# Performance work log

Measured on AMD Instinct MI355X. Metric: run time of the kernel, lower is better.

The kernel has to match this reference:

```python
import jax, jax.numpy as jnp
import numpy as np

B, D, F, E, G = 2048, 1024, 4096, 16, 2
EPS = 1e-9
LN_EPS = 1e-5


def setup_inputs() -> dict:
    key = jax.random.key(0)
    ks = jax.random.split(key, 10)
    s_in = 1.0 / np.sqrt(D)
    s_out = 1.0 / np.sqrt(F)
    return {
        "cycle_curve_data": jax.random.normal(ks[0], (B, D), jnp.float32),
        "logits": jax.random.normal(ks[1], (B, E), jnp.float32),
        "moe_masks": jax.random.randint(ks[2], (B, E), 0, 2, jnp.int32),
        "ew_in": jax.random.uniform(ks[3], (E, D, F), jnp.float32, -s_in, s_in),
        "ew_out": jax.random.uniform(ks[4], (E, F, D), jnp.float32, -s_out, s_out),
        "eb_out": jax.random.uniform(ks[5], (E, D), jnp.float32, -s_out, s_out),
        "gw_in": jax.random.uniform(ks[6], (G, D, F), jnp.float32, -s_in, s_in),
        "gw_out": jax.random.uniform(ks[7], (G, F, D), jnp.float32, -s_out, s_out),
        "gb_out": jax.random.uniform(ks[8], (G, D), jnp.float32, -s_out, s_out),
        "ln_gamma": jnp.ones((D,), jnp.float32),
        "ln_beta": jnp.zeros((D,), jnp.float32),
    }


def _moe_forward(x, logits, moe_masks, ew_in, ew_out, eb_out, gw_in, gw_out, gb_out, ln_gamma, ln_beta):
    b = x.shape[0]
    mask = (moe_masks == 1).astype(logits.dtype)          # [B,E]
    raw = jax.nn.softmax(logits, axis=1)                   # [B,E]
    gates = raw * mask
    gates = gates / (jnp.sum(gates, axis=1, keepdims=True) + EPS)
    # Per-expert MLPBlockGELU over all tokens; gate=0 zeroes out non-dispatched
    # tokens exactly as MOEDispatcher.combine does.
    h = jax.nn.gelu(jnp.einsum('bd,edf->ebf', x, ew_in), approximate=False)  # [E,B,F]
    eout = jnp.einsum('ebf,efd->ebd', h, ew_out) + eb_out[:, None, :]        # [E,B,D]
    moe_out = jnp.einsum('be,ebd->bd', gates, eout).astype(jnp.bfloat16)     # combine + bf16 cast
    # general experts (dense, added to routed output; bf16+f32 promotes to f32)
    gh = jax.nn.gelu(jnp.einsum('bd,gdf->gbf', x, gw_in), approximate=False)
    gout = jnp.einsum('gbf,gfd->gbd', gh, gw_out) + gb_out[:, None, :]       # [G,B,D]
    final = jnp.sum(gout, axis=0) + moe_out                                  # f32
    # residual + LayerNorm
    y = final + x
    mu = jnp.mean(y, axis=-1, keepdims=True)
    var = jnp.mean(jnp.square(y - mu), axis=-1, keepdims=True)
    final_out = (y - mu) * jax.lax.rsqrt(var + LN_EPS) * ln_gamma + ln_beta
    # training losses
    expert_logits = jnp.mean(raw, axis=0)                                    # [E]
    expert_sample_count = jnp.sum((gates != 0).astype(raw.dtype), axis=0) / b
    aug_loss = jnp.mean(expert_logits * expert_sample_count)
    s = jnp.sum(raw * mask) / b
    guide_loss = (1.0 - s) * (1.0 - s)
    return final_out, aug_loss, guide_loss


def reference(cycle_curve_data, logits, moe_masks, ew_in, ew_out, eb_out, gw_in, gw_out, gb_out, ln_gamma, ln_beta):
    return _moe_forward(cycle_curve_data, logits, moe_masks, ew_in, ew_out, eb_out,
                        gw_in, gw_out, gb_out, ln_gamma, ln_beta)
```

## Files before the change

kernel.cpp:

```cpp
#include <hip/hip_runtime.h>
#include <hip/hip_bf16.h>

#define B_TOK 2048
#define DDIM 1024
#define FDIM 4096
#define NE 16
#define NG 2
#define BD ((long)B_TOK * DDIM)

typedef unsigned short u16;
typedef __attribute__((ext_vector_type(8))) short bf16x8;
typedef __attribute__((ext_vector_type(4))) float f32x4;

__device__ inline u16 f2bf(float x) {
  union { float f; unsigned u; } v; v.f = x;
  return (u16)((v.u + 0x7fffu + ((v.u >> 16) & 1u)) >> 16);
}
__device__ inline float bfround(float x) {
  union { float f; unsigned u; } v; v.f = x;
  v.u = ((v.u + 0x7fffu + ((v.u >> 16) & 1u)) >> 16) << 16;
  return v.f;
}
__device__ inline float fast_erf(float x) {
  float ax = fabsf(x);
  float t = __builtin_amdgcn_rcpf(1.0f + 0.3275911f * ax);
  float poly = t * (0.254829592f + t * (-0.284496736f + t * (1.421413741f +
               t * (-1.453152027f + t * 1.061405429f))));
  float r = 1.0f - poly * __expf(-ax * ax);
  return copysignf(r, x);
}
__device__ inline float gelu_exact(float x) {
  return 0.5f * x * (1.0f + fast_erf(x * 0.70710678118654752440f));
}
__device__ inline void gload16(const void* g, void* l) {
  __builtin_amdgcn_global_load_lds((const __attribute__((address_space(1))) void*)g,
                                   (__attribute__((address_space(3))) void*)l, 16, 0, 0);
}
__device__ inline float waveSum(float v) {
  v += __shfl_down(v, 32); v += __shfl_down(v, 16); v += __shfl_down(v, 8);
  v += __shfl_down(v, 4);  v += __shfl_down(v, 2);  v += __shfl_down(v, 1);
  return v;
}

__global__ __launch_bounds__(256) void gating_kernel(
    const float* __restrict__ logits, const int* __restrict__ masks,
    float* __restrict__ gates, float* __restrict__ loss)
{
  const int b = blockIdx.x * 256 + threadIdx.x;
  const int lane = threadIdx.x & 63;
  const float* lr = logits + (long)b * NE;
  const int*   mr = masks  + (long)b * NE;
  float raw[NE]; int mk[NE];
  float mx = -1e30f;
#pragma unroll
  for (int e = 0; e < NE; ++e) { raw[e] = lr[e]; mx = fmaxf(mx, raw[e]); }
  float s = 0.f;
#pragma unroll
  for (int e = 0; e < NE; ++e) { raw[e] = expf(raw[e] - mx); s += raw[e]; }
  float inv = 1.0f / s;
#pragma unroll
  for (int e = 0; e < NE; ++e) raw[e] *= inv;
  float gs = 0.f;
#pragma unroll
  for (int e = 0; e < NE; ++e) { mk[e] = (mr[e] == 1); gs += mk[e] ? raw[e] : 0.f; }
  float ginv = 1.0f / (gs + 1e-9f);
  float* gr = gates + (long)b * NE;
#pragma unroll
  for (int e = 0; e < NE; ++e) gr[e] = (mk[e] ? raw[e] : 0.f) * ginv;
#pragma unroll
  for (int e = 0; e < NE; ++e) {
    float cs = waveSum(raw[e]);
    float cc = waveSum(mk[e] ? 1.f : 0.f);
    if (lane == 0) { atomicAdd(&loss[e], cs); atomicAdd(&loss[NE + e], cc); }
  }
  float t = waveSum(gs);
  if (lane == 0) atomicAdd(&loss[32], t);
}

__global__ void finalize_loss(const float* __restrict__ loss, float* __restrict__ out2) {
  if (threadIdx.x == 0) {
    float aug = 0.f;
    for (int e = 0; e < NE; ++e)
      aug += (loss[e] / (float)B_TOK) * (loss[NE + e] / (float)B_TOK);
    aug *= (1.0f / NE);
    float s = loss[32] / (float)B_TOK;
    out2[0] = aug;
    out2[1] = (1.f - s) * (1.f - s);
  }
}

__global__ __launch_bounds__(256) void compact_kernel(
    const int* __restrict__ masks, int* __restrict__ tok,
    int* __restrict__ pos, int* __restrict__ cnts)
{
  const int e = blockIdx.x, tid = threadIdx.x;
  const int lane = tid & 63, wave = tid >> 6;
  __shared__ int wcnt[4];
  __shared__ int runbase;
  if (tid == 0) runbase = 0;
  __syncthreads();
  for (int b0 = 0; b0 < B_TOK; b0 += 256) {
    int b = b0 + tid;
    int m = (masks[(long)b * NE + e] == 1);
    unsigned long long bal = __ballot(m);
    int pre = __popcll(bal & ((1ull << lane) - 1ull));
    if (lane == 0) wcnt[wave] = __popcll(bal);
    __syncthreads();
    int base = runbase;
    for (int w = 0; w < wave; ++w) base += wcnt[w];
    if (m) {
      int p = base + pre;
      tok[(e << 11) + p] = b;
      pos[(long)b * NE + e] = p;
    } else {
      pos[(long)b * NE + e] = -1;
    }
    __syncthreads();
    if (tid == 0) runbase += wcnt[0] + wcnt[1] + wcnt[2] + wcnt[3];
    __syncthreads();
  }
  const int cnt = runbase;
  const int cnt_pad = (cnt + 127) & ~127;
  for (int i = cnt + tid; i < cnt_pad; i += 256)
    tok[(e << 11) + i] = 0;
  if (tid == 0) { cnts[e] = cnt; cnts[NE + e] = cnt_pad; }
}

__global__ __launch_bounds__(256) void cvt_x_kernel(const float* __restrict__ x, u16* __restrict__ xb) {
  long i = ((long)blockIdx.x * 256 + threadIdx.x) * 4;
  float4 v = *(const float4*)&x[i];
  ushort4 o; o.x = f2bf(v.x); o.y = f2bf(v.y); o.z = f2bf(v.z); o.w = f2bf(v.w);
  *(ushort4*)&xb[i] = o;
}

__global__ __launch_bounds__(256) void bias_init_kernel(
    const float* __restrict__ gates, const float* __restrict__ eb,
    const float* __restrict__ gb, float* __restrict__ moe_bias, float* __restrict__ gen_p)
{
  long i = (long)blockIdx.x * 256 + threadIdx.x;
  int b = (int)(i >> 10), d = (int)(i & 1023);
  const float* gr = gates + (long)b * NE;
  float s = 0.f;
#pragma unroll
  for (int e = 0; e < NE; ++e) s += gr[e] * eb[e * DDIM + d];
  moe_bias[i] = s;
  gen_p[i] = gb[d] + gb[DDIM + d];
#pragma unroll
  for (int sl = 1; sl < 8; ++sl) gen_p[sl * BD + i] = 0.f;
}

__global__ __launch_bounds__(256) void transpose_cvt(
    const float* __restrict__ src, u16* __restrict__ dst,
    int R, int C, long sZ, long dZ)
{
  __shared__ float t[64][65];
  const float* s = src + (long)blockIdx.z * sZ;
  u16* d = dst + (long)blockIdx.z * dZ;
  const int c0 = blockIdx.x * 64, r0 = blockIdx.y * 64;
  const int tid = threadIdx.x;
#pragma unroll
  for (int it = 0; it < 4; ++it) {
    int idx = tid + it * 256;
    int r = idx >> 4, cq = (idx & 15) * 4;
    float4 v = *(const float4*)&s[(long)(r0 + r) * C + c0 + cq];
    t[r][cq] = v.x; t[r][cq + 1] = v.y; t[r][cq + 2] = v.z; t[r][cq + 3] = v.w;
  }
  __syncthreads();
#pragma unroll
  for (int it = 0; it < 4; ++it) {
    int idx = tid + it * 256;
    int c = idx >> 4, rq = (idx & 15) * 4;
    ushort4 o;
    o.x = f2bf(t[rq][c]); o.y = f2bf(t[rq+1][c]); o.z = f2bf(t[rq+2][c]); o.w = f2bf(t[rq+3][c]);
    *(ushort4*)&d[(long)(c0 + c) * R + r0 + rq] = o;
  }
}

template<int MODE>
__global__ __launch_bounds__(256) void gemm128(
    const u16* __restrict__ A, int lda, long aZ,
    const u16* __restrict__ Bm, int ldb, long bZ,
    int klen,
    u16* __restrict__ H, long hZ,
    float* __restrict__ C, long cZ,
    const int* __restrict__ tok, const int* __restrict__ cnts, int ebase)
{
  int lin = ((int)blockIdx.z * gridDim.y + blockIdx.y) * gridDim.x + blockIdx.x;
  const int T = gridDim.x * gridDim.y * gridDim.z;
  lin = (lin & 7) * (T >> 3) + (lin >> 3);
  const int bx = lin % gridDim.x;
  const int rest = lin / gridDim.x;
  const int by = rest % gridDim.y;
  const int bz = rest / gridDim.y;

  const int zi = (MODE == 2) ? (bz >> 2) : bz;
  const int ks = (MODE == 2) ? (bz & 3) * klen : 0;
  const int m0 = by * 128, n0 = bx * 128;
  if (MODE != 2 && cnts && m0 >= cnts[NE + ebase + zi]) return;

  __shared__ u16 sA[2][128 * 32];
  __shared__ u16 sB[2][128 * 32];
  const u16* Az = A + (long)zi * aZ;
  const u16* Bz = Bm + (long)zi * bZ;
  const int tid = threadIdx.x, lane = tid & 63, wave = tid >> 6;

  const int off = tid * 16;
  const int sr  = off >> 6;
  const int ske = (off & 63) >> 1;
  int arow0 = m0 + sr, arow1 = m0 + sr + 64;
  if (MODE == 0 && tok) {
    const int* tz = tok + ((ebase + zi) << 11);
    arow0 = tz[arow0]; arow1 = tz[arow1];
  }
  const u16* gA0 = Az + (long)arow0 * lda + ks + ske;
  const u16* gA1 = Az + (long)arow1 * lda + ks + ske;
  const u16* gB0 = Bz + (long)(n0 + sr) * ldb + ks + ske;
  const u16* gB1 = gB0 + (long)64 * ldb;

  const int wr = wave >> 1, wc = wave & 1;
  const int fr = lane & 15, fk = (lane >> 4) * 8;
  const int rAo = (wr * 64 + fr) * 32 + fk;
  const int rBo = (wc * 64 + fr) * 32 + fk;

  f32x4 zero = {0.f, 0.f, 0.f, 0.f};
  f32x4 acc[4][4];
#pragma unroll
  for (int m = 0; m < 4; ++m)
#pragma unroll
    for (int n = 0; n < 4; ++n) acc[m][n] = zero;

  auto STAGE = [&](int buf, int kk) {
    gload16(gA0 + kk, &sA[buf][wave * 512]);
    gload16(gA1 + kk, &sA[buf][2048 + wave * 512]);
    gload16(gB0 + kk, &sB[buf][wave * 512]);
    gload16(gB1 + kk, &sB[buf][2048 + wave * 512]);
  };
  auto COMPUTE = [&](int buf) {
    bf16x8 av[4], bv[4];
#pragma unroll
    for (int m = 0; m < 4; ++m) av[m] = *(const bf16x8*)(&sA[buf][rAo + m * 512]);
#pragma unroll
    for (int n = 0; n < 4; ++n) bv[n] = *(const bf16x8*)(&sB[buf][rBo + n * 512]);
#pragma unroll
    for (int m = 0; m < 4; ++m)
#pragma unroll
      for (int n = 0; n < 4; ++n)
        acc[m][n] = __builtin_amdgcn_mfma_f32_16x16x32_bf16(av[m], bv[n], acc[m][n], 0, 0, 0);
  };

  const int nt = klen >> 5;
  STAGE(0, 0);
  __syncthreads();
  for (int t = 0; t < nt; t += 2) {
    STAGE(1, (t + 1) << 5);
    COMPUTE(0);
    __syncthreads();
    if (t + 2 < nt) STAGE(0, (t + 2) << 5);
    COMPUTE(1);
    __syncthreads();
  }

  const int er = m0 + wr * 64 + (lane >> 4) * 4;
  const int ec = n0 + wc * 64 + fr;
  if (MODE == 0) {
    u16* Hz = H + (long)zi * hZ;
#pragma unroll
    for (int m = 0; m < 4; ++m)
#pragma unroll
      for (int n = 0; n < 4; ++n) {
        f32x4 v = acc[m][n];
        int rb = er + m * 16, cb = ec + n * 16;
#pragma unroll
        for (int j = 0; j < 4; ++j)
          Hz[(long)(rb + j) * FDIM + cb] = f2bf(gelu_exact(v[j]));
      }
  } else if (MODE == 1) {
    float* Cz = C + (long)(ebase + zi) * cZ;
#pragma unroll
    for (int m = 0; m < 4; ++m)
#pragma unroll
      for (int n = 0; n < 4; ++n) {
        f32x4 v = acc[m][n];
        int rb = er + m * 16, cb = ec + n * 16;
#pragma unroll
        for (int j = 0; j < 4; ++j)
          Cz[(long)(rb + j) * DDIM + cb] = v[j];
      }
  } else {
    float* Cz = C + (long)bz * cZ;
#pragma unroll
    for (int m = 0; m < 4; ++m)
#pragma unroll
      for (int n = 0; n < 4; ++n) {
        f32x4 v = acc[m][n];
        int rb = er + m * 16, cb = ec + n * 16;
#pragma unroll
        for (int j = 0; j < 4; ++j)
          Cz[(long)(rb + j) * DDIM + cb] += v[j];
      }
  }
}

__global__ __launch_bounds__(256) void combine_ln_kernel(
    const float* __restrict__ x, const float* __restrict__ moe_bias,
    const float* __restrict__ Eout, const float* __restrict__ gen_p,
    const int* __restrict__ pos, const float* __restrict__ gates,
    const float* __restrict__ gamma, const float* __restrict__ beta,
    float* __restrict__ out)
{
  const int b = blockIdx.x, tid = threadIdx.x;
  const int lane = tid & 63, wave = tid >> 6;
  const long base = (long)b * DDIM;
  __shared__ int posr[NE];
  __shared__ float gr[NE];
  __shared__ float red[4];
  if (tid < NE) { posr[tid] = pos[(long)b * NE + tid]; gr[tid] = gates[(long)b * NE + tid]; }
  __syncthreads();
  float y[4];
  float ls = 0.f;
#pragma unroll
  for (int i = 0; i < 4; ++i) {
    int d = tid + i * 256;
    long idx = base + d;
    float moe = moe_bias[idx];
#pragma unroll
    for (int e = 0; e < NE; ++e) {
      int p = posr[e];
      if (p >= 0) moe += gr[e] * Eout[((long)e * B_TOK + p) * DDIM + d];
    }
    moe = bfround(moe);
    float ge = 0.f;
#pragma unroll
    for (int sl = 0; sl < 8; ++sl) ge += gen_p[(long)sl * BD + idx];
    y[i] = moe + ge + x[idx];
    ls += y[i];
  }
  float t = waveSum(ls);
  if (lane == 0) red[wave] = t;
  __syncthreads();
  float mean = (red[0] + red[1] + red[2] + red[3]) * (1.0f / DDIM);
  __syncthreads();
  float vs = 0.f;
#pragma unroll
  for (int i = 0; i < 4; ++i) { float d2 = y[i] - mean; vs += d2 * d2; }
  t = waveSum(vs);
  if (lane == 0) red[wave] = t;
  __syncthreads();
  float var = (red[0] + red[1] + red[2] + red[3]) * (1.0f / DDIM);
  float inv = rsqrtf(var + 1e-5f);
#pragma unroll
  for (int i = 0; i < 4; ++i) {
    int d = tid + i * 256;
    out[base + d] = (y[i] - mean) * inv * gamma[d] + beta[d];
  }
}

extern "C" void kernel_launch(void* const* d_in, const int* in_sizes, int n_in,
                              void* d_out, int out_size, void* d_ws, size_t ws_size,
                              hipStream_t stream)
{
  const float* x      = (const float*)d_in[0];
  const float* logits = (const float*)d_in[1];
  const int*   masks  = (const int*)d_in[2];
  const float* ew_in  = (const float*)d_in[3];
  const float* ew_out = (const float*)d_in[4];
  const float* eb_out = (const float*)d_in[5];
  const float* gw_in  = (const float*)d_in[6];
  const float* gw_out = (const float*)d_in[7];
  const float* gb_out = (const float*)d_in[8];
  const float* gamma  = (const float*)d_in[9];
  const float* beta   = (const float*)d_in[10];
  float* out = (float*)d_out;

  char* w = (char*)d_ws;
  size_t off = 0;
  auto alloc = [&](size_t bytes) -> void* {
    off = (off + 4095) & ~(size_t)4095;
    void* p = w + off; off += bytes; return p;
  };
  const long DF = (long)DDIM * FDIM;
  const long BF = (long)B_TOK * FDIM;

  float* gates    = (float*)alloc((size_t)B_TOK * NE * 4);
  float* loss     = (float*)alloc(64 * 4);
  int*   tok      = (int*)alloc((size_t)NE * B_TOK * 4);
  int*   pos      = (int*)alloc((size_t)B_TOK * NE * 4);
  int*   cnts     = (int*)alloc(2 * NE * 4);
  u16*   xb       = (u16*)alloc((size_t)BD * 2);
  float* moe_bias = (float*)alloc((size_t)BD * 4);
  float* gen_p    = (float*)alloc(8 * (size_t)BD * 4);
  float* Eout     = (float*)alloc((size_t)NE * BD * 4);
  u16*   WgInT    = (u16*)alloc((size_t)NG * DF * 2);
  u16*   WgOutT   = (u16*)alloc((size_t)NG * DF * 2);
  u16*   Hg       = (u16*)alloc((size_t)NG * BF * 2);

  const size_t per = 2 * (size_t)DF * 2 + (size_t)BF * 2 + 3 * 4096;
  int CE = 16;
  while (CE > 1 && off + (size_t)CE * per > ws_size) CE >>= 1;
  u16* WinT  = (u16*)alloc((size_t)CE * DF * 2);
  u16* WoutT = (u16*)alloc((size_t)CE * DF * 2);
  u16* Hb    = (u16*)alloc((size_t)CE * BF * 2);

  hipMemsetAsync(loss, 0, 64 * 4, stream);
  gating_kernel<<<8, 256, 0, stream>>>(logits, masks, gates, loss);
  finalize_loss<<<1, 64, 0, stream>>>(loss, out + BD);
  compact_kernel<<<NE, 256, 0, stream>>>(masks, tok, pos, cnts);
  cvt_x_kernel<<<2048, 256, 0, stream>>>(x, xb);
  bias_init_kernel<<<8192, 256, 0, stream>>>(gates, eb_out, gb_out, moe_bias, gen_p);

  for (int e0 = 0; e0 < NE; e0 += CE) {
    transpose_cvt<<<dim3(FDIM/64, DDIM/64, CE), 256, 0, stream>>>(
        ew_in + (long)e0 * DF, WinT, DDIM, FDIM, DF, DF);
    transpose_cvt<<<dim3(DDIM/64, FDIM/64, CE), 256, 0, stream>>>(
        ew_out + (long)e0 * DF, WoutT, FDIM, DDIM, DF, DF);
    gemm128<0><<<dim3(FDIM/128, B_TOK/128, CE), 256, 0, stream>>>(
        xb, DDIM, 0L, WinT, DDIM, DF, DDIM,
        Hb, BF, nullptr, 0L, tok, cnts, e0);
    gemm128<1><<<dim3(DDIM/128, B_TOK/128, CE), 256, 0, stream>>>(
        Hb, FDIM, BF, WoutT, FDIM, DF, FDIM,
        nullptr, 0L, Eout, BD, nullptr, cnts, e0);
  }

  transpose_cvt<<<dim3(FDIM/64, DDIM/64, NG), 256, 0, stream>>>(
      gw_in, WgInT, DDIM, FDIM, DF, DF);
  transpose_cvt<<<dim3(DDIM/64, FDIM/64, NG), 256, 0, stream>>>(
      gw_out, WgOutT, FDIM, DDIM, DF, DF);
  gemm128<0><<<dim3(FDIM/128, B_TOK/128, NG), 256, 0, stream>>>(
      xb, DDIM, 0L, WgInT, DDIM, DF, DDIM,
      Hg, BF, nullptr, 0L, nullptr, nullptr, 0);
  gemm128<2><<<dim3(DDIM/128, B_TOK/128, NG * 4), 256, 0, stream>>>(
      Hg, FDIM, BF, WgOutT, FDIM, DF, FDIM / 4,
      nullptr, 0L, gen_p, BD, nullptr, nullptr, 0);

  combine_ln_kernel<<<B_TOK, 256, 0, stream>>>(
      x, moe_bias, Eout, gen_p, pos, gates, gamma, beta, out);
}
```

Baseline: 929.4 us.

## Triple-buffer GEMM K-loop with vmcnt waits and drop split-K zero-init

The GEMM main loop moves from a two-stage LDS double buffer with full __syncthreads to a three-stage ring buffer. Explicit s_waitcnt vmcnt and raw s_barrier calls let two tiles of global loads stay in flight during MFMA compute. Separately, the split-K general-expert GEMM now stores its partials instead of accumulating into a pre-zeroed buffer. The general bias add moves into the combine/LayerNorm kernel, which removes the large zero-fill writes from bias_init. The ring buffer uses more LDS per block and depends on nt being suitably aligned for the tail handling.

```diff
diff --git a/kernel.cpp b/kernel.cpp
--- a/kernel.cpp
+++ b/kernel.cpp
@@ -135,7 +135,7 @@
 
 __global__ __launch_bounds__(256) void bias_init_kernel(
     const float* __restrict__ gates, const float* __restrict__ eb,
-    const float* __restrict__ gb, float* __restrict__ moe_bias, float* __restrict__ gen_p)
+    float* __restrict__ moe_bias)
 {
   long i = (long)blockIdx.x * 256 + threadIdx.x;
   int b = (int)(i >> 10), d = (int)(i & 1023);
@@ -144,9 +144,6 @@
 #pragma unroll
   for (int e = 0; e < NE; ++e) s += gr[e] * eb[e * DDIM + d];
   moe_bias[i] = s;
-  gen_p[i] = gb[d] + gb[DDIM + d];
-#pragma unroll
-  for (int sl = 1; sl < 8; ++sl) gen_p[sl * BD + i] = 0.f;
 }
 
 __global__ __launch_bounds__(256) void transpose_cvt(
@@ -198,8 +195,8 @@
   const int m0 = by * 128, n0 = bx * 128;
   if (MODE != 2 && cnts && m0 >= cnts[NE + ebase + zi]) return;
 
-  __shared__ u16 sA[2][128 * 32];
-  __shared__ u16 sB[2][128 * 32];
+  __shared__ u16 sA[3][128 * 32];
+  __shared__ u16 sB[3][128 * 32];
   const u16* Az = A + (long)zi * aZ;
   const u16* Bz = Bm + (long)zi * bZ;
   const int tid = threadIdx.x, lane = tid & 63, wave = tid >> 6;
@@ -229,18 +226,19 @@
 #pragma unroll
     for (int n = 0; n < 4; ++n) acc[m][n] = zero;
 
-  auto STAGE = [&](int buf, int kk) {
-    gload16(gA0 + kk, &sA[buf][wave * 512]);
-    gload16(gA1 + kk, &sA[buf][2048 + wave * 512]);
-    gload16(gB0 + kk, &sB[buf][wave * 512]);
-    gload16(gB1 + kk, &sB[buf][2048 + wave * 512]);
+  auto STAGE = [&](u16* dA, u16* dB, int t) {
+    const int kk = t << 5;
+    gload16(gA0 + kk, dA + wave * 512);
+    gload16(gA1 + kk, dA + 2048 + wave * 512);
+    gload16(gB0 + kk, dB + wave * 512);
+    gload16(gB1 + kk, dB + 2048 + wave * 512);
   };
-  auto COMPUTE = [&](int buf) {
+  auto COMPUTE = [&](const u16* bA, const u16* bB) {
     bf16x8 av[4], bv[4];
 #pragma unroll
-    for (int m = 0; m < 4; ++m) av[m] = *(const bf16x8*)(&sA[buf][rAo + m * 512]);
-#pragma unroll
-    for (int n = 0; n < 4; ++n) bv[n] = *(const bf16x8*)(&sB[buf][rBo + n * 512]);
+    for (int m = 0; m < 4; ++m) av[m] = *(const bf16x8*)(bA + rAo + m * 512);
+#pragma unroll
+    for (int n = 0; n < 4; ++n) bv[n] = *(const bf16x8*)(bB + rBo + n * 512);
 #pragma unroll
     for (int m = 0; m < 4; ++m)
 #pragma unroll
@@ -248,17 +246,33 @@
         acc[m][n] = __builtin_amdgcn_mfma_f32_16x16x32_bf16(av[m], bv[n], acc[m][n], 0, 0, 0);
   };
 
+#define PIPE(SA, SB, KIDX, CA, CB)                                   \
+  STAGE(SA, SB, KIDX);                                               \
+  asm volatile("s_waitcnt vmcnt(8)" ::: "memory");                   \
+  __builtin_amdgcn_s_barrier();                                      \
+  asm volatile("" ::: "memory");                                     \
+  COMPUTE(CA, CB);                                                   \
+  asm volatile("" ::: "memory");                                     \
+  __builtin_amdgcn_s_barrier();                                      \
+  asm volatile("" ::: "memory");
+
   const int nt = klen >> 5;
-  STAGE(0, 0);
-  __syncthreads();
-  for (int t = 0; t < nt; t += 2) {
-    STAGE(1, (t + 1) << 5);
-    COMPUTE(0);
-    __syncthreads();
-    if (t + 2 < nt) STAGE(0, (t + 2) << 5);
-    COMPUTE(1);
-    __syncthreads();
-  }
+  STAGE(sA[0], sB[0], 0);
+  STAGE(sA[1], sB[1], 1);
+  for (int t = 0; t + 2 < nt; t += 3) {
+    PIPE(sA[2], sB[2], t + 2, sA[0], sB[0]);
+    PIPE(sA[0], sB[0], t + 3, sA[1], sB[1]);
+    PIPE(sA[1], sB[1], t + 4, sA[2], sB[2]);
+  }
+  asm volatile("s_waitcnt vmcnt(4)" ::: "memory");
+  __builtin_amdgcn_s_barrier();
+  asm volatile("" ::: "memory");
+  COMPUTE(sA[0], sB[0]);
+  asm volatile("s_waitcnt vmcnt(0)" ::: "memory");
+  __builtin_amdgcn_s_barrier();
+  asm volatile("" ::: "memory");
+  COMPUTE(sA[1], sB[1]);
+#undef PIPE
 
   const int er = m0 + wr * 64 + (lane >> 4) * 4;
   const int ec = n0 + wc * 64 + fr;
@@ -296,7 +310,7 @@
         int rb = er + m * 16, cb = ec + n * 16;
 #pragma unroll
         for (int j = 0; j < 4; ++j)
-          Cz[(long)(rb + j) * DDIM + cb] += v[j];
+          Cz[(long)(rb + j) * DDIM + cb] = v[j];
       }
   }
 }
@@ -304,6 +318,7 @@
 __global__ __launch_bounds__(256) void combine_ln_kernel(
     const float* __restrict__ x, const float* __restrict__ moe_bias,
     const float* __restrict__ Eout, const float* __restrict__ gen_p,
+    const float* __restrict__ gb,
     const int* __restrict__ pos, const float* __restrict__ gates,
     const float* __restrict__ gamma, const float* __restrict__ beta,
     float* __restrict__ out)
@@ -329,7 +344,7 @@
       if (p >= 0) moe += gr[e] * Eout[((long)e * B_TOK + p) * DDIM + d];
     }
     moe = bfround(moe);
-    float ge = 0.f;
+    float ge = gb[d] + gb[DDIM + d];
 #pragma unroll
     for (int sl = 0; sl < 8; ++sl) ge += gen_p[(long)sl * BD + idx];
     y[i] = moe + ge + x[idx];
@@ -406,7 +421,7 @@
   finalize_loss<<<1, 64, 0, stream>>>(loss, out + BD);
   compact_kernel<<<NE, 256, 0, stream>>>(masks, tok, pos, cnts);
   cvt_x_kernel<<<2048, 256, 0, stream>>>(x, xb);
-  bias_init_kernel<<<8192, 256, 0, stream>>>(gates, eb_out, gb_out, moe_bias, gen_p);
+  bias_init_kernel<<<8192, 256, 0, stream>>>(gates, eb_out, moe_bias);
 
   for (int e0 = 0; e0 < NE; e0 += CE) {
     transpose_cvt<<<dim3(FDIM/64, DDIM/64, CE), 256, 0, stream>>>(
@@ -433,5 +448,5 @@
       nullptr, 0L, gen_p, BD, nullptr, nullptr, 0);
 
   combine_ln_kernel<<<B_TOK, 256, 0, stream>>>(
-      x, moe_bias, Eout, gen_p, pos, gates, gamma, beta, out);
-}
+      x, moe_bias, Eout, gen_p, gb_out, pos, gates, gamma, beta, out);
+}
```

Result: faster. 774.2 us (-16.7%).
